# Performance work log

Measured on AMD Instinct MI355X. Metric: run time of the kernel, lower is better.

The kernel has to match this reference:

```python
import jax, jax.numpy as jnp
import numpy as np

N_MEM = 50000
MATCH_THR2 = 0.01   # squared-distance match threshold (0.1 m)
EMA = 0.5           # EMA factor for matched-descriptor update
EPS = 1e-8


def _bilinear_depth(depth, uv):
    # depth: [H, W]; uv: [M, 2] pixel coords (u = x/col, v = y/row)
    H, W = depth.shape
    u = jnp.clip(uv[:, 0], 0.0, W - 1.001)
    v = jnp.clip(uv[:, 1], 0.0, H - 1.001)
    u0 = jnp.floor(u); v0 = jnp.floor(v)
    du = u - u0; dv = v - v0
    u0i = u0.astype(jnp.int32); v0i = v0.astype(jnp.int32)
    d00 = depth[v0i, u0i]
    d01 = depth[v0i, u0i + 1]
    d10 = depth[v0i + 1, u0i]
    d11 = depth[v0i + 1, u0i + 1]
    return d00 * (1 - du) * (1 - dv) + d01 * du * (1 - dv) + d10 * (1 - du) * dv + d11 * du * dv


def pix2world(points, depth_map, pose, K):
    # points [B,M,2], depth_map [B,1,H,W], pose [B,3,4] cam->world, K [B,3,3]
    d = jax.vmap(_bilinear_depth)(depth_map[:, 0], points)            # [B,M]
    pix = jnp.concatenate([points, jnp.ones_like(points[..., :1])], -1)  # [B,M,3]
    Kinv = jnp.linalg.inv(K)
    cam = jnp.einsum('bij,bmj->bmi', Kinv, pix) * d[..., None]        # [B,M,3]
    world = jnp.einsum('bij,bmj->bmi', pose[:, :, :3], cam) + pose[:, :, 3][:, None, :]
    valid = (d > 0) & jnp.isfinite(world).all(-1)                      # [B,M]
    return world, valid


def memory_write(pts, desc, valid, mem_pts, mem_desc, next_ptr):
    # pts [P,3], desc [P,D]; mem_pts [N,3], mem_desc [N,D]
    d2 = (jnp.sum(pts * pts, -1, keepdims=True)
          - 2.0 * pts @ mem_pts.T
          + jnp.sum(mem_pts * mem_pts, -1)[None, :])                  # [P,N]
    idx = jnp.argmin(d2, axis=1)                                       # [P]
    dmin = jnp.take_along_axis(d2, idx[:, None], axis=1)[:, 0]
    match = (dmin < MATCH_THR2) & valid
    n_match = match.sum()
    # returned descriptors come from the (non-differentiable) memory buffer;
    # unmatched entries return their own descriptor (cos=1 -> zero loss/grad)
    matched_desc = jax.lax.stop_gradient(jnp.where(match[:, None], mem_desc[idx], desc))
    # --- state update (buffers: no gradient) ---
    dsg = jax.lax.stop_gradient(desc)
    psg = jax.lax.stop_gradient(pts)
    unm = (~match) & valid
    slots = (next_ptr + jnp.cumsum(unm.astype(jnp.int32)) - 1) % N_MEM
    widx = jnp.where(unm, slots, idx)                                  # [P]
    old_pts = mem_pts[widx]; old_desc = mem_desc[widx]
    upd = old_desc * EMA + dsg * (1.0 - EMA)
    upd = upd / (jnp.linalg.norm(upd, axis=-1, keepdims=True) + EPS)
    new_desc_vals = jnp.where(match[:, None], upd, jnp.where(unm[:, None], dsg, old_desc))
    new_pts_vals = jnp.where(unm[:, None], psg, old_pts)
    new_mem_desc = mem_desc.at[widx].set(new_desc_vals)
    new_mem_pts = mem_pts.at[widx].set(new_pts_vals)
    return matched_desc, n_match, new_mem_pts, new_mem_desc


def setup_inputs() -> dict:
    key = jax.random.key(0)
    ks = jax.random.split(key, 8)
    B, M, D, H, W = 8, 512, 256, 480, 640
    points = jax.random.uniform(ks[0], (B, M, 2), jnp.float32) * jnp.array([W - 2.0, H - 2.0])
    depth_map = 0.5 + 4.5 * jax.random.uniform(ks[1], (B, 1, H, W), jnp.float32)
    # proper rotations via QR + small translations
    A = np.asarray(jax.random.normal(ks[2], (B, 3, 3)))
    Rs = np.stack([np.linalg.qr(A[b])[0] for b in range(B)]).astype(np.float32)
    t = np.asarray(jax.random.normal(ks[3], (B, 3, 1))) * 2.0
    pose = jnp.asarray(np.concatenate([Rs, t.astype(np.float32)], axis=2))  # [B,3,4]
    Kmat = jnp.broadcast_to(jnp.array([[320.0, 0.0, 320.0], [0.0, 320.0, 240.0], [0.0, 0.0, 1.0]], jnp.float32), (B, 3, 3))
    descriptors = jax.random.normal(ks[4], (B, M, D), jnp.float32)
    mem_pts = (jax.random.uniform(ks[5], (N_MEM, 3), jnp.float32) - 0.5) * 16.0
    mem_desc = jax.random.normal(ks[6], (N_MEM, D), jnp.float32)
    mem_desc = mem_desc / (jnp.linalg.norm(mem_desc, axis=-1, keepdims=True) + EPS)
    return {"points": points, "depth_map": depth_map, "pose": pose, "K": Kmat,
            "descriptors": descriptors, "mem_pts": mem_pts, "mem_desc": mem_desc,
            "next_ptr": 20000}


def reference(points, depth_map, pose, K, descriptors, mem_pts, mem_desc, next_ptr):
    world, valid = pix2world(points, depth_map, pose, K)               # [B,M,3], [B,M]
    P = world.shape[0] * world.shape[1]
    pts = world.reshape(P, 3)
    desc = descriptors.reshape(P, -1)
    vmask = valid.reshape(P)
    pts = jnp.where(vmask[:, None], pts, 1e6)   # invalid points never match
    matched_desc, n_match, new_mem_pts, new_mem_desc = memory_write(
        pts, desc, vmask, mem_pts, mem_desc, next_ptr)
    a = desc / jnp.maximum(jnp.linalg.norm(desc, axis=-1, keepdims=True), EPS)
    b = matched_desc / jnp.maximum(jnp.linalg.norm(matched_desc, axis=-1, keepdims=True), EPS)
    cos = jnp.sum(a * b, -1)                                           # [P]
    nv = jnp.maximum(vmask.sum(), 1)
    loss = 1.0 - jnp.sum(cos * vmask) / nv
    return loss, n_match, new_mem_pts, new_mem_desc
```

## Files before the change

kernel.cpp:

```cpp
#include <hip/hip_runtime.h>
#include <math.h>

#define N_MEM   50000
#define P_TOT   4096
#define DDIM    256
#define HDIM    480
#define WDIM    640
#define CHUNK   196
#define DISTB   1024
#define COPYB   512
#define THR2    0.01f
#define EPSF    1e-8f
typedef unsigned long long ull;

__device__ __forceinline__ unsigned fsort(float x) {
    unsigned b = __float_as_uint(x);
    return (b & 0x80000000u) ? ~b : (b | 0x80000000u);
}

__global__ void k_world(const float* __restrict__ points,
                        const float* __restrict__ depth,
                        const float* __restrict__ pose,
                        const float* __restrict__ Kmat,
                        float4* __restrict__ pts_out,
                        int* __restrict__ flags_out,
                        ull* __restrict__ minkey)
{
    int p = blockIdx.x * 256 + threadIdx.x;
    if (p >= P_TOT) return;
    minkey[p] = 0xFFFFFFFFFFFFFFFFULL;
    int b = p >> 9;
    const float* K = Kmat + b * 9;
    float a00=K[0],a01=K[1],a02=K[2],a10=K[3],a11=K[4],a12=K[5],a20=K[6],a21=K[7],a22=K[8];
    float det = a00*(a11*a22-a12*a21) - a01*(a10*a22-a12*a20) + a02*(a10*a21-a11*a20);
    float id = 1.0f/det;
    float i00=(a11*a22-a12*a21)*id, i01=(a02*a21-a01*a22)*id, i02=(a01*a12-a02*a11)*id;
    float i10=(a12*a20-a10*a22)*id, i11=(a00*a22-a02*a20)*id, i12=(a02*a10-a00*a12)*id;
    float i20=(a10*a21-a11*a20)*id, i21=(a01*a20-a00*a21)*id, i22=(a00*a11-a01*a10)*id;

    float u = points[p*2+0], v = points[p*2+1];
    float uc = fminf(fmaxf(u, 0.f), (float)WDIM - 1.001f);
    float vc = fminf(fmaxf(v, 0.f), (float)HDIM - 1.001f);
    float u0 = floorf(uc), v0 = floorf(vc);
    float du = uc - u0, dv = vc - v0;
    int u0i = (int)u0, v0i = (int)v0;
    const float* dm = depth + (size_t)b * HDIM * WDIM;
    float d00 = dm[v0i*WDIM + u0i];
    float d01 = dm[v0i*WDIM + u0i + 1];
    float d10 = dm[(v0i+1)*WDIM + u0i];
    float d11 = dm[(v0i+1)*WDIM + u0i + 1];
    float d = d00*(1.f-du)*(1.f-dv) + d01*du*(1.f-dv) + d10*(1.f-du)*dv + d11*du*dv;

    float cx = (i00*u + i01*v + i02) * d;
    float cy = (i10*u + i11*v + i12) * d;
    float cz = (i20*u + i21*v + i22) * d;
    const float* T = pose + b * 12;
    float wx = T[0]*cx + T[1]*cy + T[2]*cz  + T[3];
    float wy = T[4]*cx + T[5]*cy + T[6]*cz  + T[7];
    float wz = T[8]*cx + T[9]*cy + T[10]*cz + T[11];
    int val = (d > 0.f) && isfinite(wx) && isfinite(wy) && isfinite(wz);
    float4 o = val ? make_float4(wx, wy, wz, 0.f) : make_float4(1e6f, 1e6f, 1e6f, 0.f);
    pts_out[p] = o;
    flags_out[p] = val;
}

__global__ __launch_bounds__(256) void k_main(const float4* __restrict__ pts,
                                              const float* __restrict__ mem_pts,
                                              const float* __restrict__ mem_desc,
                                              ull* __restrict__ minkey,
                                              float* __restrict__ out_pts,
                                              float* __restrict__ out_desc)
{
    __shared__ float4 sm[CHUNK];
    int bid = blockIdx.x;
    int t = threadIdx.x;
    if (bid < DISTB) {
        int pb = bid >> 8;
        int ch = bid & 255;
        int j0 = ch * CHUNK;
        int cnt = min(CHUNK, N_MEM - j0);
        if (t < cnt) {
            float mx = mem_pts[(j0 + t) * 3 + 0];
            float my = mem_pts[(j0 + t) * 3 + 1];
            float mz = mem_pts[(j0 + t) * 3 + 2];
            sm[t] = make_float4(mx, my, mz, mx*mx + my*my + mz*mz);
        }
        __syncthreads();
        int p0 = pb * 1024 + t;
        float4 P0 = pts[p0], P1 = pts[p0+256], P2 = pts[p0+512], P3 = pts[p0+768];
        float pp0 = P0.x*P0.x + P0.y*P0.y + P0.z*P0.z;
        float pp1 = P1.x*P1.x + P1.y*P1.y + P1.z*P1.z;
        float pp2 = P2.x*P2.x + P2.y*P2.y + P2.z*P2.z;
        float pp3 = P3.x*P3.x + P3.y*P3.y + P3.z*P3.z;
        float bd0 = 3.4e38f, bd1 = 3.4e38f, bd2 = 3.4e38f, bd3 = 3.4e38f;
        int bi0 = 0, bi1 = 0, bi2 = 0, bi3 = 0;
        for (int j = 0; j < cnt; ++j) {
            float4 mv = sm[j];
            float dot0 = P0.x*mv.x + P0.y*mv.y + P0.z*mv.z;
            float dot1 = P1.x*mv.x + P1.y*mv.y + P1.z*mv.z;
            float dot2 = P2.x*mv.x + P2.y*mv.y + P2.z*mv.z;
            float dot3 = P3.x*mv.x + P3.y*mv.y + P3.z*mv.z;
            float d0 = pp0 - 2.f*dot0 + mv.w;
            float d1 = pp1 - 2.f*dot1 + mv.w;
            float d2 = pp2 - 2.f*dot2 + mv.w;
            float d3 = pp3 - 2.f*dot3 + mv.w;
            if (d0 < bd0) { bd0 = d0; bi0 = j0 + j; }
            if (d1 < bd1) { bd1 = d1; bi1 = j0 + j; }
            if (d2 < bd2) { bd2 = d2; bi2 = j0 + j; }
            if (d3 < bd3) { bd3 = d3; bi3 = j0 + j; }
        }
        atomicMin(&minkey[p0],       ((ull)fsort(bd0) << 32) | (unsigned)bi0);
        atomicMin(&minkey[p0 + 256], ((ull)fsort(bd1) << 32) | (unsigned)bi1);
        atomicMin(&minkey[p0 + 512], ((ull)fsort(bd2) << 32) | (unsigned)bi2);
        atomicMin(&minkey[p0 + 768], ((ull)fsort(bd3) << 32) | (unsigned)bi3);
    } else {
        const long tid = (long)(bid - DISTB) * 256 + t;
        const long stride = (long)COPYB * 256;
        const float2* ds = (const float2*)mem_desc;
        float2* dd = (float2*)out_desc;
        const long ND2 = (long)N_MEM * DDIM / 2;
        long k = tid * 4;
        const long stride4 = stride * 4;
        for (; k + 3 < ND2; k += stride4) {
            float2 a0 = ds[k+0], a1 = ds[k+1], a2 = ds[k+2], a3 = ds[k+3];
            dd[k+0] = a0; dd[k+1] = a1; dd[k+2] = a2; dd[k+3] = a3;
        }
        for (; k < ND2; ++k) dd[k] = ds[k];
        const float2* ps = (const float2*)mem_pts;
        float2* pd = (float2*)out_pts;
        for (long i = tid; i < (long)N_MEM * 3 / 2; i += stride) pd[i] = ps[i];
    }
}

__global__ __launch_bounds__(256) void k_scan(const ull* __restrict__ minkey,
                                              int* __restrict__ flags,
                                              const int* __restrict__ next_ptr,
                                              int* __restrict__ widx,
                                              int* __restrict__ winner,
                                              float* __restrict__ dout)
{
    __shared__ int su[256];
    __shared__ int smc[256];
    int t = threadIdx.x;
    int base = t * 16;
    const ull thr_key = ((ull)fsort(THR2)) << 32;
    int um[16], iv[16], wvv[16];
    int usum = 0, msum = 0;
    for (int k = 0; k < 16; k++) {
        ull key = minkey[base + k];
        int v = flags[base + k] & 1;
        int m = (key < thr_key) && v;
        int u = (!m) && v;
        iv[k] = (int)(key & 0xffffffffULL);
        um[k] = u; usum += u; msum += m;
        flags[base + k] = v | (m << 1) | (u << 2);
    }
    su[t] = usum; smc[t] = msum;
    __syncthreads();
    for (int off = 1; off < 256; off <<= 1) {
        int a = su[t], b = (t >= off) ? su[t - off] : 0;
        int c = smc[t], d = (t >= off) ? smc[t - off] : 0;
        __syncthreads();
        su[t] = a + b; smc[t] = c + d;
        __syncthreads();
    }
    int excl = su[t] - usum;
    int np_ = *next_ptr;
    int run = excl;
    for (int k = 0; k < 16; k++) {
        int wv;
        if (um[k]) { run += 1; wv = (np_ + run - 1) % N_MEM; }
        else       { wv = iv[k]; }
        widx[base + k] = wv;
        wvv[k] = wv;
        winner[wv] = -1;
    }
    __syncthreads();
    for (int k = 0; k < 16; k++)
        atomicMax(&winner[wvv[k]], base + k);
    if (t == 255) dout[1] = (float)smc[255];
}

__global__ __launch_bounds__(256) void k_scatloss(const int* __restrict__ widx,
                                                  const int* __restrict__ flags,
                                                  const int* __restrict__ winner,
                                                  const float* __restrict__ desc,
                                                  const float4* __restrict__ pts,
                                                  const float* __restrict__ mem_pts,
                                                  const float* __restrict__ mem_desc,
                                                  float* __restrict__ out_pts,
                                                  float* __restrict__ out_desc,
                                                  float* __restrict__ cos_ws)
{
    __shared__ float red[16];
    int p = blockIdx.x;
    int t = threadIdx.x;
    int f = flags[p];
    int v = f & 1, m = (f >> 1) & 1, u = (f >> 2) & 1;
    int wi = widx[p];
    int win = (winner[wi] == p);
    if (!m && !win) {
        if (t == 0) cos_ws[p] = v ? 1.f : 0.f;
        return;
    }
    float dsg = desc[p * DDIM + t];
    float old = mem_desc[(long)wi * DDIM + t];
    float val, cosv;
    if (m) {
        float up = old * 0.5f + dsg * 0.5f;
        float sdd = dsg * dsg, smm2 = old * old, sdm = dsg * old, suu = up * up;
        for (int off = 32; off; off >>= 1) {
            sdd  += __shfl_xor(sdd,  off);
            smm2 += __shfl_xor(smm2, off);
            sdm  += __shfl_xor(sdm,  off);
            suu  += __shfl_xor(suu,  off);
        }
        int w = t >> 6;
        if ((t & 63) == 0) { red[w] = sdd; red[4+w] = smm2; red[8+w] = sdm; red[12+w] = suu; }
        __syncthreads();
        float dd  = red[0] + red[1] + red[2] + red[3];
        float mm2 = red[4] + red[5] + red[6] + red[7];
        float dm  = red[8] + red[9] + red[10] + red[11];
        float uu  = red[12] + red[13] + red[14] + red[15];
        cosv = dm / (fmaxf(sqrtf(dd), EPSF) * fmaxf(sqrtf(mm2), EPSF));
        val = up / (sqrtf(uu) + EPSF);
    } else {
        cosv = v ? 1.f : 0.f;
        val = u ? dsg : old;
    }
    if (win) {
        out_desc[(long)wi * DDIM + t] = val;
        if (t == 0) {
            float px, py, pz;
            if (u) { float4 P = pts[p]; px = P.x; py = P.y; pz = P.z; }
            else   { px = mem_pts[wi*3]; py = mem_pts[wi*3+1]; pz = mem_pts[wi*3+2]; }
            out_pts[wi*3+0] = px; out_pts[wi*3+1] = py; out_pts[wi*3+2] = pz;
        }
    }
    if (t == 0) cos_ws[p] = cosv;
}

__global__ __launch_bounds__(256) void k_final(const float* __restrict__ cos_ws,
                                               const int* __restrict__ flags,
                                               float* __restrict__ dout)
{
    __shared__ float ss[256];
    __shared__ float sv[256];
    int t = threadIdx.x;
    float s = 0.f, v = 0.f;
    for (int k = t; k < P_TOT; k += 256) {
        s += cos_ws[k];
        v += (float)(flags[k] & 1);
    }
    ss[t] = s; sv[t] = v;
    __syncthreads();
    for (int off = 128; off; off >>= 1) {
        if (t < off) { ss[t] += ss[t + off]; sv[t] += sv[t + off]; }
        __syncthreads();
    }
    if (t == 0) {
        float nv = fmaxf(sv[0], 1.f);
        dout[0] = 1.f - ss[0] / nv;
    }
}

extern "C" void kernel_launch(void* const* d_in, const int* in_sizes, int n_in,
                              void* d_out, int out_size, void* d_ws, size_t ws_size,
                              hipStream_t stream)
{
    const float* points   = (const float*)d_in[0];
    const float* depth    = (const float*)d_in[1];
    const float* pose     = (const float*)d_in[2];
    const float* Kmat     = (const float*)d_in[3];
    const float* desc     = (const float*)d_in[4];
    const float* mem_pts  = (const float*)d_in[5];
    const float* mem_desc = (const float*)d_in[6];
    const int*   next_ptr = (const int*)d_in[7];

    float* out      = (float*)d_out;
    float* out_pts  = out + 2;
    float* out_desc = out + 2 + (long)N_MEM * 3;

    char* ws = (char*)d_ws;
    float4* pts_ws  = (float4*)(ws);
    int* flags_ws   = (int*)(ws + 65536);
    int* widx_ws    = (int*)(ws + 81920);
    int* winner_ws  = (int*)(ws + 98304);
    float* cos_ws   = (float*)(ws + 298304);
    ull* minkey_ws  = (ull*)(ws + 314688);

    k_world   <<<16, 256, 0, stream>>>(points, depth, pose, Kmat, pts_ws, flags_ws, minkey_ws);
    k_main    <<<DISTB + COPYB, 256, 0, stream>>>(pts_ws, mem_pts, mem_desc, minkey_ws,
                                                  out_pts, out_desc);
    k_scan    <<<1, 256, 0, stream>>>(minkey_ws, flags_ws, next_ptr,
                                      widx_ws, winner_ws, out);
    k_scatloss<<<P_TOT, 256, 0, stream>>>(widx_ws, flags_ws, winner_ws, desc, pts_ws,
                                          mem_pts, mem_desc, out_pts, out_desc, cos_ws);
    k_final   <<<1, 256, 0, stream>>>(cos_ws, flags_ws, out);
}
```

Measured before the change: 176.9 us.

## Replace brute-force nearest-neighbour search with uniform-grid spatial hashing

Memory points are now binned into a 24^3 uniform grid by a histogram, prefix-scan and scatter pass. Each query then searches only the cells within the match radius, instead of scanning all 50000 memory points. The world-point projection is fused into the query blocks of the main kernel, which removes a separate launch. A global fallback key reproduces the argmin for invalid points. This removes most of the O(P·N) distance work but adds several small serial kernels, a memset, and search time that depends on how points are distributed over the grid.

Result: slower. 220.3 us (+24.5%).

```diff
diff --git a/kernel.cpp b/kernel.cpp
--- a/kernel.cpp
+++ b/kernel.cpp
@@ -6,11 +6,18 @@
 #define DDIM    256
 #define HDIM    480
 #define WDIM    640
-#define CHUNK   196
-#define DISTB   1024
+#define QB      16
 #define COPYB   512
 #define THR2    0.01f
 #define EPSF    1e-8f
+
+#define GDIM    24
+#define NCELL   13824
+#define GORG    -8.25f
+#define GINV    (1.0f/0.6875f)
+#define GRS     0.15f
+#define CPT     14
+
 typedef unsigned long long ull;
 
 __device__ __forceinline__ unsigned fsort(float x) {
@@ -18,103 +25,171 @@
     return (b & 0x80000000u) ? ~b : (b | 0x80000000u);
 }
 
-__global__ void k_world(const float* __restrict__ points,
-                        const float* __restrict__ depth,
-                        const float* __restrict__ pose,
-                        const float* __restrict__ Kmat,
-                        float4* __restrict__ pts_out,
-                        int* __restrict__ flags_out,
-                        ull* __restrict__ minkey)
-{
-    int p = blockIdx.x * 256 + threadIdx.x;
-    if (p >= P_TOT) return;
-    minkey[p] = 0xFFFFFFFFFFFFFFFFULL;
-    int b = p >> 9;
-    const float* K = Kmat + b * 9;
-    float a00=K[0],a01=K[1],a02=K[2],a10=K[3],a11=K[4],a12=K[5],a20=K[6],a21=K[7],a22=K[8];
-    float det = a00*(a11*a22-a12*a21) - a01*(a10*a22-a12*a20) + a02*(a10*a21-a11*a20);
-    float id = 1.0f/det;
-    float i00=(a11*a22-a12*a21)*id, i01=(a02*a21-a01*a22)*id, i02=(a01*a12-a02*a11)*id;
-    float i10=(a12*a20-a10*a22)*id, i11=(a00*a22-a02*a20)*id, i12=(a02*a10-a00*a12)*id;
-    float i20=(a10*a21-a11*a20)*id, i21=(a01*a20-a00*a21)*id, i22=(a00*a11-a01*a10)*id;
-
-    float u = points[p*2+0], v = points[p*2+1];
-    float uc = fminf(fmaxf(u, 0.f), (float)WDIM - 1.001f);
-    float vc = fminf(fmaxf(v, 0.f), (float)HDIM - 1.001f);
-    float u0 = floorf(uc), v0 = floorf(vc);
-    float du = uc - u0, dv = vc - v0;
-    int u0i = (int)u0, v0i = (int)v0;
-    const float* dm = depth + (size_t)b * HDIM * WDIM;
-    float d00 = dm[v0i*WDIM + u0i];
-    float d01 = dm[v0i*WDIM + u0i + 1];
-    float d10 = dm[(v0i+1)*WDIM + u0i];
-    float d11 = dm[(v0i+1)*WDIM + u0i + 1];
-    float d = d00*(1.f-du)*(1.f-dv) + d01*du*(1.f-dv) + d10*(1.f-du)*dv + d11*du*dv;
-
-    float cx = (i00*u + i01*v + i02) * d;
-    float cy = (i10*u + i11*v + i12) * d;
-    float cz = (i20*u + i21*v + i22) * d;
-    const float* T = pose + b * 12;
-    float wx = T[0]*cx + T[1]*cy + T[2]*cz  + T[3];
-    float wy = T[4]*cx + T[5]*cy + T[6]*cz  + T[7];
-    float wz = T[8]*cx + T[9]*cy + T[10]*cz + T[11];
-    int val = (d > 0.f) && isfinite(wx) && isfinite(wy) && isfinite(wz);
-    float4 o = val ? make_float4(wx, wy, wz, 0.f) : make_float4(1e6f, 1e6f, 1e6f, 0.f);
-    pts_out[p] = o;
-    flags_out[p] = val;
-}
-
-__global__ __launch_bounds__(256) void k_main(const float4* __restrict__ pts,
+__device__ __forceinline__ int cell1d(float x) {
+    int c = (int)((x - GORG) * GINV);
+    return min(max(c, 0), GDIM - 1);
+}
+
+__global__ __launch_bounds__(256) void k_hist(const float* __restrict__ mem_pts,
+                                              int* __restrict__ cell_count)
+{
+    int j = blockIdx.x * 256 + threadIdx.x;
+    if (j >= N_MEM) return;
+    float mx = mem_pts[j*3+0], my = mem_pts[j*3+1], mz = mem_pts[j*3+2];
+    int c = (cell1d(mz) * GDIM + cell1d(my)) * GDIM + cell1d(mx);
+    atomicAdd(&cell_count[c], 1);
+}
+
+__global__ __launch_bounds__(1024) void k_prefix(const int* __restrict__ cnt,
+                                                 int* __restrict__ cstart,
+                                                 int* __restrict__ ccur,
+                                                 ull* __restrict__ minkey_inv)
+{
+    __shared__ int s[1024];
+    int t = threadIdx.x;
+    if (t == 0) *minkey_inv = 0xFFFFFFFFFFFFFFFFULL;
+    int base = t * CPT;
+    int loc[CPT];
+    int sum = 0;
+    for (int i = 0; i < CPT; ++i) {
+        int idx = base + i;
+        int c = (idx < NCELL) ? cnt[idx] : 0;
+        loc[i] = sum; sum += c;
+    }
+    s[t] = sum;
+    __syncthreads();
+    for (int off = 1; off < 1024; off <<= 1) {
+        int a = s[t];
+        int b = (t >= off) ? s[t - off] : 0;
+        __syncthreads();
+        s[t] = a + b;
+        __syncthreads();
+    }
+    int ex = s[t] - sum;
+    for (int i = 0; i < CPT; ++i) {
+        int idx = base + i;
+        if (idx < NCELL) { int v = ex + loc[i]; cstart[idx] = v; ccur[idx] = v; }
+    }
+}
+
+__global__ __launch_bounds__(256) void k_scatter(const float* __restrict__ mem_pts,
+                                                 int* __restrict__ ccur,
+                                                 int* __restrict__ sorted_idx,
+                                                 ull* __restrict__ minkey_inv)
+{
+    __shared__ ull sred[4];
+    int t = threadIdx.x;
+    int j = blockIdx.x * 256 + t;
+    ull key = 0xFFFFFFFFFFFFFFFFULL;
+    if (j < N_MEM) {
+        float mx = mem_pts[j*3+0], my = mem_pts[j*3+1], mz = mem_pts[j*3+2];
+        int c = (cell1d(mz) * GDIM + cell1d(my)) * GDIM + cell1d(mx);
+        int pos = atomicAdd(&ccur[c], 1);
+        sorted_idx[pos] = j;
+        float px = 1e6f;
+        float pp  = px*px + px*px + px*px;
+        float dot = px*mx + px*my + px*mz;
+        float mm  = mx*mx + my*my + mz*mz;
+        float d   = pp - 2.f*dot + mm;
+        key = ((ull)fsort(d) << 32) | (unsigned)j;
+    }
+    for (int off = 32; off; off >>= 1) {
+        ull o = __shfl_xor(key, off);
+        key = o < key ? o : key;
+    }
+    if ((t & 63) == 0) sred[t >> 6] = key;
+    __syncthreads();
+    if (t == 0) {
+        ull a = sred[0] < sred[1] ? sred[0] : sred[1];
+        ull b = sred[2] < sred[3] ? sred[2] : sred[3];
+        ull m = a < b ? a : b;
+        atomicMin(minkey_inv, m);
+    }
+}
+
+__global__ __launch_bounds__(256) void k_main(const float* __restrict__ points,
+                                              const float* __restrict__ depth,
+                                              const float* __restrict__ pose,
+                                              const float* __restrict__ Kmat,
+                                              const int* __restrict__ cstart,
+                                              const int* __restrict__ ccount,
+                                              const int* __restrict__ sorted_idx,
                                               const float* __restrict__ mem_pts,
                                               const float* __restrict__ mem_desc,
+                                              float4* __restrict__ pts_out,
+                                              int* __restrict__ flags_out,
                                               ull* __restrict__ minkey,
                                               float* __restrict__ out_pts,
                                               float* __restrict__ out_desc)
 {
-    __shared__ float4 sm[CHUNK];
     int bid = blockIdx.x;
     int t = threadIdx.x;
-    if (bid < DISTB) {
-        int pb = bid >> 8;
-        int ch = bid & 255;
-        int j0 = ch * CHUNK;
-        int cnt = min(CHUNK, N_MEM - j0);
-        if (t < cnt) {
-            float mx = mem_pts[(j0 + t) * 3 + 0];
-            float my = mem_pts[(j0 + t) * 3 + 1];
-            float mz = mem_pts[(j0 + t) * 3 + 2];
-            sm[t] = make_float4(mx, my, mz, mx*mx + my*my + mz*mz);
+    if (bid < QB) {
+        int p = bid * 256 + t;
+        int b = p >> 9;
+        const float* K = Kmat + b * 9;
+        float a00=K[0],a01=K[1],a02=K[2],a10=K[3],a11=K[4],a12=K[5],a20=K[6],a21=K[7],a22=K[8];
+        float det = a00*(a11*a22-a12*a21) - a01*(a10*a22-a12*a20) + a02*(a10*a21-a11*a20);
+        float id = 1.0f/det;
+        float i00=(a11*a22-a12*a21)*id, i01=(a02*a21-a01*a22)*id, i02=(a01*a12-a02*a11)*id;
+        float i10=(a12*a20-a10*a22)*id, i11=(a00*a22-a02*a20)*id, i12=(a02*a10-a00*a12)*id;
+        float i20=(a10*a21-a11*a20)*id, i21=(a01*a20-a00*a21)*id, i22=(a00*a11-a01*a10)*id;
+
+        float u = points[p*2+0], v = points[p*2+1];
+        float uc = fminf(fmaxf(u, 0.f), (float)WDIM - 1.001f);
+        float vc = fminf(fmaxf(v, 0.f), (float)HDIM - 1.001f);
+        float u0 = floorf(uc), v0 = floorf(vc);
+        float du = uc - u0, dv = vc - v0;
+        int u0i = (int)u0, v0i = (int)v0;
+        const float* dm = depth + (size_t)b * HDIM * WDIM;
+        float d00 = dm[v0i*WDIM + u0i];
+        float d01 = dm[v0i*WDIM + u0i + 1];
+        float d10 = dm[(v0i+1)*WDIM + u0i];
+        float d11 = dm[(v0i+1)*WDIM + u0i + 1];
+        float d = d00*(1.f-du)*(1.f-dv) + d01*du*(1.f-dv) + d10*(1.f-du)*dv + d11*du*dv;
+
+        float cx = (i00*u + i01*v + i02) * d;
+        float cy = (i10*u + i11*v + i12) * d;
+        float cz = (i20*u + i21*v + i22) * d;
+        const float* T = pose + b * 12;
+        float wx = T[0]*cx + T[1]*cy + T[2]*cz  + T[3];
+        float wy = T[4]*cx + T[5]*cy + T[6]*cz  + T[7];
+        float wz = T[8]*cx + T[9]*cy + T[10]*cz + T[11];
+        int val = (d > 0.f) && isfinite(wx) && isfinite(wy) && isfinite(wz);
+        float px = val ? wx : 1e6f;
+        float py = val ? wy : 1e6f;
+        float pz = val ? wz : 1e6f;
+        pts_out[p] = make_float4(px, py, pz, 0.f);
+        flags_out[p] = val;
+
+        ull best = 0xFFFFFFFFFFFFFFFFULL;
+        if (val) {
+            float pp = px*px + py*py + pz*pz;
+            int cx0 = cell1d(px - GRS), cx1 = cell1d(px + GRS);
+            int cy0 = cell1d(py - GRS), cy1 = cell1d(py + GRS);
+            int cz0 = cell1d(pz - GRS), cz1 = cell1d(pz + GRS);
+            for (int zz = cz0; zz <= cz1; ++zz)
+                for (int yy = cy0; yy <= cy1; ++yy) {
+                    int rowc = (zz * GDIM + yy) * GDIM;
+                    for (int xx = cx0; xx <= cx1; ++xx) {
+                        int cell = rowc + xx;
+                        int s0 = cstart[cell];
+                        int n  = ccount[cell];
+                        for (int k = s0; k < s0 + n; ++k) {
+                            int j = sorted_idx[k];
+                            float mx = mem_pts[j*3+0], my = mem_pts[j*3+1], mz = mem_pts[j*3+2];
+                            float mm  = mx*mx + my*my + mz*mz;
+                            float dot = px*mx + py*my + pz*mz;
+                            float dd2 = pp - 2.f*dot + mm;
+                            ull key = ((ull)fsort(dd2) << 32) | (unsigned)j;
+                            best = key < best ? key : best;
+                        }
+                    }
+                }
         }
-        __syncthreads();
-        int p0 = pb * 1024 + t;
-        float4 P0 = pts[p0], P1 = pts[p0+256], P2 = pts[p0+512], P3 = pts[p0+768];
-        float pp0 = P0.x*P0.x + P0.y*P0.y + P0.z*P0.z;
-        float pp1 = P1.x*P1.x + P1.y*P1.y + P1.z*P1.z;
-        float pp2 = P2.x*P2.x + P2.y*P2.y + P2.z*P2.z;
-        float pp3 = P3.x*P3.x + P3.y*P3.y + P3.z*P3.z;
-        float bd0 = 3.4e38f, bd1 = 3.4e38f, bd2 = 3.4e38f, bd3 = 3.4e38f;
-        int bi0 = 0, bi1 = 0, bi2 = 0, bi3 = 0;
-        for (int j = 0; j < cnt; ++j) {
-            float4 mv = sm[j];
-            float dot0 = P0.x*mv.x + P0.y*mv.y + P0.z*mv.z;
-            float dot1 = P1.x*mv.x + P1.y*mv.y + P1.z*mv.z;
-            float dot2 = P2.x*mv.x + P2.y*mv.y + P2.z*mv.z;
-            float dot3 = P3.x*mv.x + P3.y*mv.y + P3.z*mv.z;
-            float d0 = pp0 - 2.f*dot0 + mv.w;
-            float d1 = pp1 - 2.f*dot1 + mv.w;
-            float d2 = pp2 - 2.f*dot2 + mv.w;
-            float d3 = pp3 - 2.f*dot3 + mv.w;
-            if (d0 < bd0) { bd0 = d0; bi0 = j0 + j; }
-            if (d1 < bd1) { bd1 = d1; bi1 = j0 + j; }
-            if (d2 < bd2) { bd2 = d2; bi2 = j0 + j; }
-            if (d3 < bd3) { bd3 = d3; bi3 = j0 + j; }
-        }
-        atomicMin(&minkey[p0],       ((ull)fsort(bd0) << 32) | (unsigned)bi0);
-        atomicMin(&minkey[p0 + 256], ((ull)fsort(bd1) << 32) | (unsigned)bi1);
-        atomicMin(&minkey[p0 + 512], ((ull)fsort(bd2) << 32) | (unsigned)bi2);
-        atomicMin(&minkey[p0 + 768], ((ull)fsort(bd3) << 32) | (unsigned)bi3);
+        minkey[p] = best;
     } else {
-        const long tid = (long)(bid - DISTB) * 256 + t;
+        const long tid = (long)(bid - QB) * 256 + t;
         const long stride = (long)COPYB * 256;
         const float2* ds = (const float2*)mem_desc;
         float2* dd = (float2*)out_desc;
@@ -135,6 +210,7 @@
 __global__ __launch_bounds__(256) void k_scan(const ull* __restrict__ minkey,
                                               int* __restrict__ flags,
                                               const int* __restrict__ next_ptr,
+                                              const ull* __restrict__ minkey_inv,
                                               int* __restrict__ widx,
                                               int* __restrict__ winner,
                                               float* __restrict__ dout)
@@ -144,11 +220,12 @@
     int t = threadIdx.x;
     int base = t * 16;
     const ull thr_key = ((ull)fsort(THR2)) << 32;
+    ull inv = *minkey_inv;
     int um[16], iv[16], wvv[16];
     int usum = 0, msum = 0;
     for (int k = 0; k < 16; k++) {
-        ull key = minkey[base + k];
         int v = flags[base + k] & 1;
+        ull key = v ? minkey[base + k] : inv;
         int m = (key < thr_key) && v;
         int u = (!m) && v;
         iv[k] = (int)(key & 0xffffffffULL);
@@ -282,17 +359,28 @@
     float* out_desc = out + 2 + (long)N_MEM * 3;
 
     char* ws = (char*)d_ws;
-    float4* pts_ws  = (float4*)(ws);
-    int* flags_ws   = (int*)(ws + 65536);
-    int* widx_ws    = (int*)(ws + 81920);
-    int* winner_ws  = (int*)(ws + 98304);
-    float* cos_ws   = (float*)(ws + 298304);
-    ull* minkey_ws  = (ull*)(ws + 314688);
-
-    k_world   <<<16, 256, 0, stream>>>(points, depth, pose, Kmat, pts_ws, flags_ws, minkey_ws);
-    k_main    <<<DISTB + COPYB, 256, 0, stream>>>(pts_ws, mem_pts, mem_desc, minkey_ws,
-                                                  out_pts, out_desc);
-    k_scan    <<<1, 256, 0, stream>>>(minkey_ws, flags_ws, next_ptr,
+    float4* pts_ws   = (float4*)(ws);
+    int* flags_ws    = (int*)(ws + 65536);
+    int* widx_ws     = (int*)(ws + 81920);
+    int* winner_ws   = (int*)(ws + 98304);
+    float* cos_ws    = (float*)(ws + 298304);
+    ull* minkey_ws   = (ull*)(ws + 314688);
+    int* cell_count  = (int*)(ws + 347456);
+    int* cell_start  = (int*)(ws + 402752);
+    int* cell_cursor = (int*)(ws + 458048);
+    int* sorted_idx  = (int*)(ws + 513344);
+    ull* minkey_inv  = (ull*)(ws + 713344);
+
+    hipMemsetAsync(cell_count, 0, NCELL * sizeof(int), stream);
+    k_hist    <<<196, 256, 0, stream>>>(mem_pts, cell_count);
+    k_prefix  <<<1, 1024, 0, stream>>>(cell_count, cell_start, cell_cursor, minkey_inv);
+    k_scatter <<<196, 256, 0, stream>>>(mem_pts, cell_cursor, sorted_idx, minkey_inv);
+    k_main    <<<QB + COPYB, 256, 0, stream>>>(points, depth, pose, Kmat,
+                                               cell_start, cell_count, sorted_idx,
+                                               mem_pts, mem_desc,
+                                               pts_ws, flags_ws, minkey_ws,
+                                               out_pts, out_desc);
+    k_scan    <<<1, 256, 0, stream>>>(minkey_ws, flags_ws, next_ptr, minkey_inv,
                                       widx_ws, winner_ws, out);
     k_scatloss<<<P_TOT, 256, 0, stream>>>(widx_ws, flags_ws, winner_ws, desc, pts_ws,
                                           mem_pts, mem_desc, out_pts, out_desc, cos_ws);
```
